# Performance work log

Hardware: AMD Instinct MI355X
Metric: run time of the kernel (lower is better)

The kernel has to match this reference:

```python
import jax, jax.numpy as jnp
import numpy as np

D_MODEL = 1024
N_HEADS = 16
D_HEAD = D_MODEL // N_HEADS


def setup_inputs() -> dict:
    key = jax.random.key(0)
    ks = jax.random.split(key, 5)
    B, T = 2, 2048
    x = jax.random.normal(ks[0], (B, T, D_MODEL), dtype=jnp.float32)
    s = 1.0 / np.sqrt(D_MODEL)
    W_qkv = jax.random.normal(ks[1], (D_MODEL, 3 * D_MODEL), dtype=jnp.float32) * s
    b_qkv = jnp.zeros((3 * D_MODEL,), dtype=jnp.float32)
    W_proj = jax.random.normal(ks[2], (D_MODEL, D_MODEL), dtype=jnp.float32) * s
    b_proj = jnp.zeros((D_MODEL,), dtype=jnp.float32)
    return {"x": x, "W_qkv": W_qkv, "b_qkv": b_qkv, "W_proj": W_proj, "b_proj": b_proj}


def reference(x, W_qkv, b_qkv, W_proj, b_proj):
    B, T, C = x.shape
    qkv = x @ W_qkv + b_qkv                      # [B,T,3C]
    q, k, v = jnp.split(qkv, 3, axis=-1)
    # [B,T,C] -> [B,H,T,Dh]
    def to_heads(t):
        return t.reshape(B, T, N_HEADS, D_HEAD).transpose(0, 2, 1, 3)
    q, k, v = to_heads(q), to_heads(k), to_heads(v)
    scale = 1.0 / np.sqrt(D_HEAD).astype(np.float32)
    scores = jnp.einsum('bhqd,bhkd->bhqk', q, k) * scale  # [B,H,T,T]
    causal = jnp.tril(jnp.ones((T, T), dtype=bool))
    scores = jnp.where(causal, scores, -jnp.inf)
    attn = jax.nn.softmax(scores, axis=-1)
    out = jnp.einsum('bhqk,bhkd->bhqd', attn, v)          # [B,H,T,Dh]
    out = out.transpose(0, 2, 1, 3).reshape(B, T, C)
    return out @ W_proj + b_proj
```

## Files before the change

### kernel.cpp

```cpp
#include <hip/hip_runtime.h>
#include <hip/hip_bf16.h>
#include <cstdint>


using u16 = unsigned short;
using u32 = unsigned int;

typedef __bf16 bf16x8 __attribute__((ext_vector_type(8)));
typedef float f32x4 __attribute__((ext_vector_type(4)));

#define AS1 __attribute__((address_space(1)))
#define AS3 __attribute__((address_space(3)))

__device__ __forceinline__ u16 f2bf(float f) {
  u32 u = __float_as_uint(f);
  u += 0x7fffu + ((u >> 16) & 1u);
  return (u16)(u >> 16);
}
__device__ __forceinline__ u32 cvtpk(float a, float b) {
  u32 r;
  asm("v_cvt_pk_bf16_f32 %0, %1, %2" : "=v"(r) : "v"(a), "v"(b));
  return r;
}

__global__ __launch_bounds__(256) void prep(const float* __restrict__ x,
                                            u16* __restrict__ xb,
                                            const float* __restrict__ W0,
                                            u16* __restrict__ T0,
                                            const float* __restrict__ W1,
                                            u16* __restrict__ T1) {
  const int bx = blockIdx.x;
  const int tid = threadIdx.x;
  if (bx < 4096) {
    const int i = bx * 256 + tid;
    float4 v = ((const float4*)x)[i];
    ushort4 o;
    o.x = f2bf(v.x); o.y = f2bf(v.y); o.z = f2bf(v.z); o.w = f2bf(v.w);
    ((ushort4*)xb)[i] = o;
    return;
  }
  __shared__ float t[32][33];
  const int idx = bx - 4096;
  const int bxx = idx & 127, by = idx >> 7;
  const float* W; u16* Wt; int N, n0;
  if (bxx < 96) { W = W0; Wt = T0; N = 3072; n0 = bxx * 32; }
  else          { W = W1; Wt = T1; N = 1024; n0 = (bxx - 96) * 32; }
  const int k0 = by * 32;
  const int tx = tid & 31, ty = tid >> 5;
#pragma unroll
  for (int i = 0; i < 4; ++i)
    t[ty + i * 8][tx] = W[(size_t)(k0 + ty + i * 8) * N + n0 + tx];
  __syncthreads();
#pragma unroll
  for (int i = 0; i < 4; ++i)
    Wt[(size_t)(n0 + ty + i * 8) * 1024 + k0 + tx] = f2bf(t[tx][ty + i * 8]);
}

#define MFMA16 __builtin_amdgcn_mfma_f32_16x16x32_bf16

__global__ __launch_bounds__(512, 2) void gemm_qkv(const u16* __restrict__ A,
                                                   const u16* __restrict__ Bt,
                                                   const float* __restrict__ bias,
                                                   u16* __restrict__ qb,
                                                   u16* __restrict__ KF,
                                                   u16* __restrict__ VF,
                                                   float sc_val) {
  constexpr int NT = 16;
  constexpr int BUFO = 7 * 4096;
  __shared__ __align__(16) u16 sm[2 * BUFO];

  const int tid  = threadIdx.x;
  const int lane = tid & 63;
  const int w    = tid >> 6;
  const int quad = lane >> 4;
  const int l15  = lane & 15;

  const int bid = blockIdx.x;
  const int xcd = bid & 7, c = bid >> 3;
  const int mt = (xcd >> 1) * 4 + (c & 3);
  const int nt = (xcd & 1) * 8 + (c >> 2);
  const int bm = mt * 256, bn = nt * 192;

  const int wr = (w >> 2) * 128;
  const int wc = (w & 3) * 48;

  const int srow = tid >> 3;
  const int scol = (((tid & 7) ^ ((tid >> 3) & 7)) << 3);

#define STAGEA(ch, ktile, bufo)                                                 \
  __builtin_amdgcn_global_load_lds(                                             \
      (AS1 const void*)(A + (size_t)(bm + (ch) * 64 + srow) * 1024 +            \
                        ((ktile) << 6) + scol),                                 \
      (AS3 void*)(sm + (bufo) + (ch) * 4096 + tid * 8), 16, 0, 0)
#define STAGEB(ch, ktile, bufo)                                                 \
  __builtin_amdgcn_global_load_lds(                                             \
      (AS1 const void*)(Bt + (size_t)(bn + (ch) * 64 + srow) * 1024 +           \
                        ((ktile) << 6) + scol),                                 \
      (AS3 void*)(sm + (bufo) + (4 + (ch)) * 4096 + tid * 8), 16, 0, 0)

  const int ca = (w >> 2) * 2;
  int abase_lo[4], abase_hi[4], bbase[3];
#pragma unroll
  for (int mi = 0; mi < 4; ++mi) {
    abase_lo[mi] = (ca + 0) * 4096 + (mi * 16 + l15) * 64;
    abase_hi[mi] = (ca + 1) * 4096 + (mi * 16 + l15) * 64;
  }
#pragma unroll
  for (int ni = 0; ni < 3; ++ni) {
    const int rb = wc + ni * 16 + l15;
    bbase[ni] = (4 + (rb >> 6)) * 4096 + (rb & 63) * 64;
  }
  const int sw0 = ((quad ^ (l15 & 7)) << 3);
  const int sw1 = sw0 ^ 32;

  STAGEA(0, 0, 0); STAGEA(1, 0, 0); STAGEA(2, 0, 0); STAGEA(3, 0, 0);
  STAGEB(0, 0, 0); STAGEB(1, 0, 0); STAGEB(2, 0, 0);
  STAGEB(0, 1, BUFO); STAGEB(1, 1, BUFO);
  STAGEB(2, 1, BUFO); STAGEA(0, 1, BUFO); STAGEA(1, 1, BUFO);
  asm volatile("s_waitcnt vmcnt(5)" ::: "memory");
  __builtin_amdgcn_s_barrier();

  f32x4 acc[8][3] = {};
  bf16x8 alo[4][2], ahi[4][2], b[3][2];

#pragma unroll 2
  for (int j = 0; j < NT; ++j) {
    const int bo  = (j & 1) * BUFO;
    const int nbo = bo ^ BUFO;
    const u16* smb = sm + bo;

#pragma unroll
    for (int mi = 0; mi < 4; ++mi) {
      alo[mi][0] = *(const bf16x8*)(smb + abase_lo[mi] + sw0);
      alo[mi][1] = *(const bf16x8*)(smb + abase_lo[mi] + sw1);
    }
#pragma unroll
    for (int ni = 0; ni < 2; ++ni) {
      b[ni][0] = *(const bf16x8*)(smb + bbase[ni] + sw0);
      b[ni][1] = *(const bf16x8*)(smb + bbase[ni] + sw1);
    }
    if (j + 1 < NT) { STAGEA(2, j + 1, nbo); STAGEA(3, j + 1, nbo); }
    __builtin_amdgcn_s_barrier();
    asm volatile("s_waitcnt lgkmcnt(0)" ::: "memory");
    __builtin_amdgcn_s_setprio(1);
#pragma unroll
    for (int mi = 0; mi < 4; ++mi)
#pragma unroll
      for (int ni = 0; ni < 2; ++ni) {
        acc[mi][ni] = MFMA16(alo[mi][0], b[ni][0], acc[mi][ni], 0, 0, 0);
        acc[mi][ni] = MFMA16(alo[mi][1], b[ni][1], acc[mi][ni], 0, 0, 0);
      }
    __builtin_amdgcn_s_setprio(0);
    __builtin_amdgcn_s_barrier();

#pragma unroll
    for (int mi = 0; mi < 4; ++mi) {
      ahi[mi][0] = *(const bf16x8*)(smb + abase_hi[mi] + sw0);
      ahi[mi][1] = *(const bf16x8*)(smb + abase_hi[mi] + sw1);
    }
    b[2][0] = *(const bf16x8*)(smb + bbase[2] + sw0);
    b[2][1] = *(const bf16x8*)(smb + bbase[2] + sw1);
    if (j + 2 < NT) { STAGEB(0, j + 2, bo); STAGEB(1, j + 2, bo); }
    __builtin_amdgcn_s_barrier();
    asm volatile("s_waitcnt lgkmcnt(0)" ::: "memory");
    __builtin_amdgcn_s_setprio(1);
#pragma unroll
    for (int mi = 0; mi < 4; ++mi) {
      acc[mi][2] = MFMA16(alo[mi][0], b[2][0], acc[mi][2], 0, 0, 0);
      acc[mi][2] = MFMA16(alo[mi][1], b[2][1], acc[mi][2], 0, 0, 0);
      acc[4 + mi][0] = MFMA16(ahi[mi][0], b[0][0], acc[4 + mi][0], 0, 0, 0);
      acc[4 + mi][0] = MFMA16(ahi[mi][1], b[0][1], acc[4 + mi][0], 0, 0, 0);
    }
    __builtin_amdgcn_s_setprio(0);
    __builtin_amdgcn_s_barrier();

    if (j + 2 < NT) { STAGEB(2, j + 2, bo); STAGEA(0, j + 2, bo); STAGEA(1, j + 2, bo); }
    __builtin_amdgcn_s_barrier();
    __builtin_amdgcn_s_setprio(1);
#pragma unroll
    for (int mi = 0; mi < 4; ++mi)
#pragma unroll
      for (int ni = 1; ni < 3; ++ni) {
        acc[4 + mi][ni] = MFMA16(ahi[mi][0], b[ni][0], acc[4 + mi][ni], 0, 0, 0);
        acc[4 + mi][ni] = MFMA16(ahi[mi][1], b[ni][1], acc[4 + mi][ni], 0, 0, 0);
      }
    __builtin_amdgcn_s_setprio(0);
    if (j + 2 < NT)
      asm volatile("s_waitcnt vmcnt(5)" ::: "memory");
    else
      asm volatile("s_waitcnt vmcnt(0)" ::: "memory");
    __builtin_amdgcn_s_barrier();
  }
#undef STAGEA
#undef STAGEB

  const int crow0 = bm + wr + (quad << 2);
  const int ccol0 = bn + wc + l15;
#pragma unroll
  for (int ni = 0; ni < 3; ++ni) {
    const int n = ccol0 + ni * 16;
    const float bv = bias[n];
    if (n < 1024) {
#pragma unroll
      for (int mi = 0; mi < 8; ++mi) {
        const int m0 = crow0 + mi * 16;
#pragma unroll
        for (int r = 0; r < 4; ++r)
          qb[(size_t)(m0 + r) * 1024 + n] = f2bf((acc[mi][ni][r] + bv) * sc_val);
      }
    } else if (n < 2048) {
      const int hk = (n - 1024) >> 6;
      const int d  = (n - 1024) & 63;
      const int hh = d >> 5, qd = (d >> 3) & 3, jj = d & 7;
#pragma unroll
      for (int mi = 0; mi < 8; ++mi) {
#pragma unroll
        for (int r = 0; r < 4; ++r) {
          const int t  = crow0 + mi * 16 + r;
          const int bb = t >> 11, tt = t & 2047;
          const int kt = tt >> 6, mm = (tt >> 4) & 3, l = tt & 15;
          KF[((size_t)((bb * 16 + hk) * 32 + kt) * 8 + mm * 2 + hh) * 512 +
             (qd * 16 + l) * 8 + jj] = f2bf(acc[mi][ni][r] + bv);
        }
      }
    } else {
      const int hv = (n - 2048) >> 6;
      const int d  = (n - 2048) & 63;
      const int di = d >> 4, l = d & 15;
#pragma unroll
      for (int mi = 0; mi < 8; ++mi) {
#pragma unroll
        for (int r = 0; r < 4; ++r) {
          const int t  = crow0 + mi * 16 + r;
          const int bb = t >> 11, tt = t & 2047;
          const int kt = tt >> 6, to = tt & 63;
          const int mq = to >> 4, qd2 = (to >> 2) & 3, rr = to & 3;
          const int hh = mq >> 1, jj = (mq & 1) * 4 + rr;
          VF[((size_t)((bb * 16 + hv) * 32 + kt) * 8 + hh * 4 + di) * 512 +
             (qd2 * 16 + l) * 8 + jj] = f2bf(acc[mi][ni][r] + bv);
        }
      }
    }
  }
}

__global__ __launch_bounds__(256) void gemm_proj(const u16* __restrict__ A,
                                                 const u16* __restrict__ Bt,
                                                 const float* __restrict__ bias,
                                                 float* __restrict__ C) {
  constexpr int BM = 128, BN = 64, BK = 32;
  constexpr int K = 1024, N = 1024;
  __shared__ __align__(16) u16 lA[BM * BK];
  __shared__ __align__(16) u16 lB[BN * BK];
  const int tid  = threadIdx.x;
  const int lane = tid & 63;
  const int wave = tid >> 6;
  const int bm = blockIdx.x * BM;
  const int bn = blockIdx.y * BN;
  const int wr = wave * 32;

  f32x4 acc[2][4] = {};

  const int f0 = (wave << 10) + (lane << 4);
  const int f1 = f0 + 4096;
  const int ar0 = f0 >> 6, ac0 = (f0 & 63) >> 1;
  const int ar1 = f1 >> 6, ac1 = (f1 & 63) >> 1;

  const int arow = wr + (lane & 15);
  const int brow = (lane & 15);
  const int kk   = (lane >> 4) << 3;

  for (int k0 = 0; k0 < K; k0 += BK) {
    __builtin_amdgcn_global_load_lds((AS1 const void*)(A + (size_t)(bm + ar0) * K + k0 + ac0),
                                     (AS3 void*)(lA + (wave << 9)), 16, 0, 0);
    __builtin_amdgcn_global_load_lds((AS1 const void*)(A + (size_t)(bm + ar1) * K + k0 + ac1),
                                     (AS3 void*)(lA + ((wave + 4) << 9)), 16, 0, 0);
    __builtin_amdgcn_global_load_lds((AS1 const void*)(Bt + (size_t)(bn + ar0) * K + k0 + ac0),
                                     (AS3 void*)(lB + (wave << 9)), 16, 0, 0);
    __syncthreads();

    bf16x8 af[2], bfr[4];
#pragma unroll
    for (int mi = 0; mi < 2; ++mi)
      af[mi] = *(const bf16x8*)&lA[(arow + mi * 16) * BK + kk];
#pragma unroll
    for (int ni = 0; ni < 4; ++ni)
      bfr[ni] = *(const bf16x8*)&lB[(brow + ni * 16) * BK + kk];
#pragma unroll
    for (int mi = 0; mi < 2; ++mi)
#pragma unroll
      for (int ni = 0; ni < 4; ++ni)
        acc[mi][ni] = __builtin_amdgcn_mfma_f32_16x16x32_bf16(af[mi], bfr[ni],
                                                              acc[mi][ni], 0, 0, 0);
    __syncthreads();
  }

  const int crow0 = bm + wr + ((lane >> 4) << 2);
  const int ccol0 = bn + (lane & 15);
#pragma unroll
  for (int ni = 0; ni < 4; ++ni) {
    const int n = ccol0 + ni * 16;
    const float bv = bias[n];
#pragma unroll
    for (int mi = 0; mi < 2; ++mi) {
      const int m0 = crow0 + mi * 16;
#pragma unroll
      for (int r = 0; r < 4; ++r)
        C[(size_t)(m0 + r) * N + n] = acc[mi][ni][r] + bv;
    }
  }
}

__global__ __launch_bounds__(128, 2) void attn_bal(const u16* __restrict__ qb,
                                                   const u16* __restrict__ KF,
                                                   const u16* __restrict__ VF,
                                                   u16* __restrict__ out) {
  const int bid = blockIdx.x;
  const int c   = bid >> 3;
  const int u   = c & 31;
  const int bh  = (bid & 7) | ((c >> 5) << 3);
  const int b = bh >> 4, h = bh & 15;
  const int tid = threadIdx.x;
  const int lane = tid & 63;
  const int par  = tid >> 6;
  const int quad = lane >> 4;
  const int l15  = lane & 15;

  __shared__ float CB[64][41];

  const u16* qbase = qb + (size_t)b * 2048 * 1024 + h * 64;
  const size_t fb = (size_t)bh * 32 * 4096 + lane * 8;
  const u16* kfb = KF + fb;
  const u16* vfb = VF + fb;

  union { u32 u4[4]; bf16x8 v; } onesu;
  onesu.u4[0] = onesu.u4[1] = onesu.u4[2] = onesu.u4[3] = 0x3f803f80u;
  const bf16x8 onesf = onesu.v;

  u16* const outb = out + (size_t)b * 2048 * 1024 + h * 64 + l15;

  auto run_group = [&](int g32) {
    const int q0 = g32 * 32;
    const int ktmax = g32 >> 1;

    bf16x8 qf[2][2];
#pragma unroll
    for (int g = 0; g < 2; ++g)
#pragma unroll
      for (int hh = 0; hh < 2; ++hh)
        qf[g][hh] = *(const bf16x8*)(qbase + (size_t)(q0 + g * 16 + l15) * 1024 +
                                     hh * 32 + quad * 8);

    f32x4 accO[2][4] = {};
    f32x4 accL[2] = {};

    bf16x8 kA[4][2], kB[4][2], vA[2][4], vB[2][4];
    {
      const u16* kp = kfb + (size_t)par * 4096;
      const u16* vp = vfb + (size_t)par * 4096;
#pragma unroll
      for (int m = 0; m < 4; ++m)
#pragma unroll
        for (int hh = 0; hh < 2; ++hh)
          kA[m][hh] = *(const bf16x8*)(kp + (m * 2 + hh) * 512);
#pragma unroll
      for (int hh = 0; hh < 2; ++hh)
#pragma unroll
        for (int di = 0; di < 4; ++di)
          vA[hh][di] = *(const bf16x8*)(vp + (hh * 4 + di) * 512);
    }

    auto tile = [&](int kt, bf16x8 (&KC)[4][2], bf16x8 (&KN)[4][2],
                    bf16x8 (&VC)[2][4], bf16x8 (&VN)[2][4]) {
      const int ktn = (kt + 2 <= ktmax) ? kt + 2 : ktmax;
      const u16* kpn = kfb + (size_t)ktn * 4096;
      const u16* vpn = vfb + (size_t)ktn * 4096;
#pragma unroll
      for (int m = 0; m < 4; ++m)
#pragma unroll
        for (int hh = 0; hh < 2; ++hh)
          KN[m][hh] = *(const bf16x8*)(kpn + (m * 2 + hh) * 512);
#pragma unroll
      for (int hh = 0; hh < 2; ++hh)
#pragma unroll
        for (int di = 0; di < 4; ++di)
          VN[hh][di] = *(const bf16x8*)(vpn + (hh * 4 + di) * 512);

      const bool diag = (kt == ktmax);
      bf16x8 ap[2][2];
#pragma unroll
      for (int g = 0; g < 2; ++g) {
        f32x4 sT[4] = {};
#pragma unroll
        for (int m = 0; m < 4; ++m) {
          sT[m] = MFMA16(KC[m][0], qf[g][0], sT[m], 0, 0, 0);
          sT[m] = MFMA16(KC[m][1], qf[g][1], sT[m], 0, 0, 0);
        }
        float pv[4][4];
        if (diag) {
          const int qgl = q0 + g * 16 + l15;
#pragma unroll
          for (int m = 0; m < 4; ++m)
#pragma unroll
            for (int r = 0; r < 4; ++r) {
              const bool msk = (kt * 64 + m * 16 + quad * 4 + r) > qgl;
              pv[m][r] = msk ? 0.f : __builtin_amdgcn_exp2f(sT[m][r]);
            }
        } else {
#pragma unroll
          for (int m = 0; m < 4; ++m)
#pragma unroll
            for (int r = 0; r < 4; ++r)
              pv[m][r] = __builtin_amdgcn_exp2f(sT[m][r]);
        }
        union { u32 u4[4]; bf16x8 v; } t0, t1;
        t0.u4[0] = cvtpk(pv[0][0], pv[0][1]);
        t0.u4[1] = cvtpk(pv[0][2], pv[0][3]);
        t0.u4[2] = cvtpk(pv[1][0], pv[1][1]);
        t0.u4[3] = cvtpk(pv[1][2], pv[1][3]);
        t1.u4[0] = cvtpk(pv[2][0], pv[2][1]);
        t1.u4[1] = cvtpk(pv[2][2], pv[2][3]);
        t1.u4[2] = cvtpk(pv[3][0], pv[3][1]);
        t1.u4[3] = cvtpk(pv[3][2], pv[3][3]);
        ap[g][0] = t0.v;
        ap[g][1] = t1.v;
      }

#pragma unroll
      for (int hh = 0; hh < 2; ++hh)
#pragma unroll
        for (int di = 0; di < 4; ++di) {
          bf16x8 bv = VC[hh][di];
#pragma unroll
          for (int g = 0; g < 2; ++g)
            accO[g][di] = MFMA16(ap[g][hh], bv, accO[g][di], 0, 0, 0);
        }
#pragma unroll
      for (int g = 0; g < 2; ++g) {
        accL[g] = MFMA16(ap[g][0], onesf, accL[g], 0, 0, 0);
        accL[g] = MFMA16(ap[g][1], onesf, accL[g], 0, 0, 0);
      }
    };

    for (int kt = par; kt <= ktmax; ) {
      tile(kt, kA, kB, vA, vB); kt += 2;
      if (kt > ktmax) break;
      tile(kt, kB, kA, vB, vA); kt += 2;
    }

    if (par) {
      float* cb = CB[lane];
#pragma unroll
      for (int g = 0; g < 2; ++g) {
#pragma unroll
        for (int di = 0; di < 4; ++di)
#pragma unroll
          for (int r = 0; r < 4; ++r)
            cb[g * 16 + di * 4 + r] = accO[g][di][r];
#pragma unroll
        for (int r = 0; r < 4; ++r)
          cb[32 + g * 4 + r] = accL[g][r];
      }
    }
    __syncthreads();
    if (!par) {
      const float* cb = CB[lane];
#pragma unroll
      for (int g = 0; g < 2; ++g) {
#pragma unroll
        for (int di = 0; di < 4; ++di)
#pragma unroll
          for (int r = 0; r < 4; ++r)
            accO[g][di][r] += cb[g * 16 + di * 4 + r];
#pragma unroll
        for (int r = 0; r < 4; ++r)
          accL[g][r] += cb[32 + g * 4 + r];
      }
#pragma unroll
      for (int g = 0; g < 2; ++g)
#pragma unroll
        for (int r = 0; r < 4; ++r) {
          const float inv = 1.f / accL[g][r];
          const int q = q0 + g * 16 + quad * 4 + r;
          u16* op = outb + (size_t)q * 1024;
#pragma unroll
          for (int di = 0; di < 4; ++di)
            op[di * 16] = f2bf(accO[g][di][r] * inv);
        }
    }
    __syncthreads();
  };

  run_group(63 - u);
  run_group(u);
}

extern "C" void kernel_launch(void* const* d_in, const int* in_sizes, int n_in,
                              void* d_out, int out_size, void* d_ws, size_t ws_size,
                              hipStream_t stream) {
  const float* x     = (const float*)d_in[0];
  const float* Wqkv  = (const float*)d_in[1];
  const float* bqkv  = (const float*)d_in[2];
  const float* Wproj = (const float*)d_in[3];
  const float* bproj = (const float*)d_in[4];
  float* out = (float*)d_out;

  char* ws = (char*)d_ws;
  u16* xb     = (u16*)(ws);
  u16* wqkvT  = (u16*)(ws + 8388608);
  u16* wprojT = (u16*)(ws + 14680064);
  u16* qb     = (u16*)(ws + 16777216);
  u16* KF     = (u16*)(ws + 25165824);
  u16* VF     = (u16*)(ws + 33554432);
  u16* att    = (u16*)(ws + 41943040);

  constexpr float cs = 0.18033688011f;

  prep<<<8192, 256, 0, stream>>>(x, xb, Wqkv, wqkvT, Wproj, wprojT);

  gemm_qkv<<<dim3(256), 512, 0, stream>>>(xb, wqkvT, bqkv, qb, KF, VF, cs);

  attn_bal<<<dim3(1024), 128, 0, stream>>>(qb, KF, VF, att);

  gemm_proj<<<dim3(32, 16), 256, 0, stream>>>(att, wprojT, bproj, out);
}
```

Measured before the change: 159.3 us.

## Rewrite projection GEMM with 128x128 tiles, double-buffered swizzled LDS and XCD mapping

The output projection GEMM moves from 128x64 tiles with BK=32 and a single LDS buffer to 128x128 tiles with BK=64. It double-buffers LDS with asynchronous global-to-LDS prefetch and XOR-swizzles the LDS layout to avoid bank conflicts. The launch becomes a 1D grid remapped so neighbouring M tiles share an XCD, and MFMA sections are split into halves interleaved with loads under raised wave priority. This targets load latency and synchronisation stalls in the projection, at the cost of fewer blocks (256) and more registers per thread.

```diff
diff --git a/kernel.cpp b/kernel.cpp
--- a/kernel.cpp
+++ b/kernel.cpp
@@ -244,69 +244,140 @@
   }
 }
 
-__global__ __launch_bounds__(256) void gemm_proj(const u16* __restrict__ A,
-                                                 const u16* __restrict__ Bt,
-                                                 const float* __restrict__ bias,
-                                                 float* __restrict__ C) {
-  constexpr int BM = 128, BN = 64, BK = 32;
-  constexpr int K = 1024, N = 1024;
-  __shared__ __align__(16) u16 lA[BM * BK];
-  __shared__ __align__(16) u16 lB[BN * BK];
+__global__ __launch_bounds__(256, 2) void gemm_proj(const u16* __restrict__ A,
+                                                    const u16* __restrict__ Bt,
+                                                    const float* __restrict__ bias,
+                                                    float* __restrict__ C) {
+  constexpr int NT = 16;
+  constexpr int BUFO = 4 * 4096;
+  __shared__ __align__(16) u16 sm[2 * BUFO];
+
   const int tid  = threadIdx.x;
   const int lane = tid & 63;
-  const int wave = tid >> 6;
-  const int bm = blockIdx.x * BM;
-  const int bn = blockIdx.y * BN;
-  const int wr = wave * 32;
-
-  f32x4 acc[2][4] = {};
-
-  const int f0 = (wave << 10) + (lane << 4);
-  const int f1 = f0 + 4096;
-  const int ar0 = f0 >> 6, ac0 = (f0 & 63) >> 1;
-  const int ar1 = f1 >> 6, ac1 = (f1 & 63) >> 1;
-
-  const int arow = wr + (lane & 15);
-  const int brow = (lane & 15);
-  const int kk   = (lane >> 4) << 3;
-
-  for (int k0 = 0; k0 < K; k0 += BK) {
-    __builtin_amdgcn_global_load_lds((AS1 const void*)(A + (size_t)(bm + ar0) * K + k0 + ac0),
-                                     (AS3 void*)(lA + (wave << 9)), 16, 0, 0);
-    __builtin_amdgcn_global_load_lds((AS1 const void*)(A + (size_t)(bm + ar1) * K + k0 + ac1),
-                                     (AS3 void*)(lA + ((wave + 4) << 9)), 16, 0, 0);
-    __builtin_amdgcn_global_load_lds((AS1 const void*)(Bt + (size_t)(bn + ar0) * K + k0 + ac0),
-                                     (AS3 void*)(lB + (wave << 9)), 16, 0, 0);
-    __syncthreads();
-
-    bf16x8 af[2], bfr[4];
-#pragma unroll
-    for (int mi = 0; mi < 2; ++mi)
-      af[mi] = *(const bf16x8*)&lA[(arow + mi * 16) * BK + kk];
-#pragma unroll
-    for (int ni = 0; ni < 4; ++ni)
-      bfr[ni] = *(const bf16x8*)&lB[(brow + ni * 16) * BK + kk];
-#pragma unroll
-    for (int mi = 0; mi < 2; ++mi)
-#pragma unroll
-      for (int ni = 0; ni < 4; ++ni)
-        acc[mi][ni] = __builtin_amdgcn_mfma_f32_16x16x32_bf16(af[mi], bfr[ni],
-                                                              acc[mi][ni], 0, 0, 0);
-    __syncthreads();
-  }
-
-  const int crow0 = bm + wr + ((lane >> 4) << 2);
-  const int ccol0 = bn + (lane & 15);
+  const int w    = tid >> 6;
+  const int quad = lane >> 4;
+  const int l15  = lane & 15;
+
+  const int bid = blockIdx.x;
+  const int xcd = bid & 7, c = bid >> 3;
+  const int mt = xcd * 4 + (c & 3);
+  const int nt = c >> 2;
+  const int bm = mt * 128, bn = nt * 128;
+
+  const int wr = (w >> 1) * 64;
+  const int wcC = (w & 1) * 64;
+
+  const int srow = tid >> 3;
+  const int scol = (((tid & 7) ^ ((tid >> 3) & 7)) << 3);
+
+#define PSTAGEA(ch, ktile, bufo)                                                \
+  do {                                                                          \
+    const u16* _s = A + (size_t)(bm + (ch) * 64 + srow) * 1024 +                \
+                    ((ktile) << 6) + scol;                                      \
+    u16* _d = sm + (bufo) + (ch) * 4096 + tid * 8;                              \
+    __builtin_amdgcn_global_load_lds((AS1 const void*)_s, (AS3 void*)_d,        \
+                                     16, 0, 0);                                 \
+    __builtin_amdgcn_global_load_lds((AS1 const void*)(_s + (32 << 10)),        \
+                                     (AS3 void*)(_d + 2048), 16, 0, 0);         \
+  } while (0)
+#define PSTAGEB(ch, ktile, bufo)                                                \
+  do {                                                                          \
+    const u16* _s = Bt + (size_t)(bn + (ch) * 64 + srow) * 1024 +               \
+                    ((ktile) << 6) + scol;                                      \
+    u16* _d = sm + (bufo) + (2 + (ch)) * 4096 + tid * 8;                        \
+    __builtin_amdgcn_global_load_lds((AS1 const void*)_s, (AS3 void*)_d,        \
+                                     16, 0, 0);                                 \
+    __builtin_amdgcn_global_load_lds((AS1 const void*)(_s + (32 << 10)),        \
+                                     (AS3 void*)(_d + 2048), 16, 0, 0);         \
+  } while (0)
+
+  int abase[4], bbase[4];
+#pragma unroll
+  for (int mi = 0; mi < 4; ++mi)
+    abase[mi] = (w >> 1) * 4096 + (mi * 16 + l15) * 64;
+#pragma unroll
+  for (int ni = 0; ni < 4; ++ni)
+    bbase[ni] = (2 + (w & 1)) * 4096 + (ni * 16 + l15) * 64;
+  const int sw0 = ((quad ^ (l15 & 7)) << 3);
+  const int sw1 = sw0 ^ 32;
+
+  PSTAGEA(0, 0, 0); PSTAGEA(1, 0, 0);
+  PSTAGEB(0, 0, 0); PSTAGEB(1, 0, 0);
+  PSTAGEA(0, 1, BUFO); PSTAGEA(1, 1, BUFO);
+  asm volatile("s_waitcnt vmcnt(4)" ::: "memory");
+  __builtin_amdgcn_s_barrier();
+
+  f32x4 acc[4][4] = {};
+  bf16x8 a[4][2], b[4][2];
+
+#pragma unroll 2
+  for (int j = 0; j < NT; ++j) {
+    const int bo  = (j & 1) * BUFO;
+    const int nbo = bo ^ BUFO;
+    const u16* smb = sm + bo;
+
+#pragma unroll
+    for (int mi = 0; mi < 4; ++mi) {
+      a[mi][0] = *(const bf16x8*)(smb + abase[mi] + sw0);
+      a[mi][1] = *(const bf16x8*)(smb + abase[mi] + sw1);
+    }
+#pragma unroll
+    for (int ni = 0; ni < 2; ++ni) {
+      b[ni][0] = *(const bf16x8*)(smb + bbase[ni] + sw0);
+      b[ni][1] = *(const bf16x8*)(smb + bbase[ni] + sw1);
+    }
+    if (j + 1 < NT) { PSTAGEB(0, j + 1, nbo); PSTAGEB(1, j + 1, nbo); }
+    __builtin_amdgcn_s_barrier();
+    asm volatile("s_waitcnt lgkmcnt(0)" ::: "memory");
+    __builtin_amdgcn_s_setprio(1);
+#pragma unroll
+    for (int mi = 0; mi < 4; ++mi)
+#pragma unroll
+      for (int ni = 0; ni < 2; ++ni) {
+        acc[mi][ni] = MFMA16(a[mi][0], b[ni][0], acc[mi][ni], 0, 0, 0);
+        acc[mi][ni] = MFMA16(a[mi][1], b[ni][1], acc[mi][ni], 0, 0, 0);
+      }
+    __builtin_amdgcn_s_setprio(0);
+    __builtin_amdgcn_s_barrier();
+
+#pragma unroll
+    for (int ni = 2; ni < 4; ++ni) {
+      b[ni][0] = *(const bf16x8*)(smb + bbase[ni] + sw0);
+      b[ni][1] = *(const bf16x8*)(smb + bbase[ni] + sw1);
+    }
+    if (j + 2 < NT) { PSTAGEA(0, j + 2, bo); PSTAGEA(1, j + 2, bo); }
+    __builtin_amdgcn_s_barrier();
+    asm volatile("s_waitcnt lgkmcnt(0)" ::: "memory");
+    __builtin_amdgcn_s_setprio(1);
+#pragma unroll
+    for (int mi = 0; mi < 4; ++mi)
+#pragma unroll
+      for (int ni = 2; ni < 4; ++ni) {
+        acc[mi][ni] = MFMA16(a[mi][0], b[ni][0], acc[mi][ni], 0, 0, 0);
+        acc[mi][ni] = MFMA16(a[mi][1], b[ni][1], acc[mi][ni], 0, 0, 0);
+      }
+    __builtin_amdgcn_s_setprio(0);
+    if (j + 2 < NT)
+      asm volatile("s_waitcnt vmcnt(4)" ::: "memory");
+    else
+      asm volatile("s_waitcnt vmcnt(0)" ::: "memory");
+    __builtin_amdgcn_s_barrier();
+  }
+#undef PSTAGEA
+#undef PSTAGEB
+
+  const int crow0 = bm + wr + (quad << 2);
+  const int ccol0 = bn + wcC + l15;
 #pragma unroll
   for (int ni = 0; ni < 4; ++ni) {
     const int n = ccol0 + ni * 16;
     const float bv = bias[n];
 #pragma unroll
-    for (int mi = 0; mi < 2; ++mi) {
+    for (int mi = 0; mi < 4; ++mi) {
       const int m0 = crow0 + mi * 16;
 #pragma unroll
       for (int r = 0; r < 4; ++r)
-        C[(size_t)(m0 + r) * N + n] = acc[mi][ni][r] + bv;
+        C[(size_t)(m0 + r) * 1024 + n] = acc[mi][ni][r] + bv;
     }
   }
 }
@@ -522,5 +593,5 @@
 
   attn_bal<<<dim3(1024), 128, 0, stream>>>(qb, KF, VF, att);
 
-  gemm_proj<<<dim3(32, 16), 256, 0, stream>>>(att, wprojT, bproj, out);
-}
+  gemm_proj<<<dim3(256), 256, 0, stream>>>(att, wprojT, bproj, out);
+}
```

Result: no change. 156.2 us (-1.9%).
